# Kernel optimization log

Hardware: AMD Instinct MI355X
Metric: run time of the kernel (lower is better)

The kernel has to match this reference:

```python
import jax, jax.numpy as jnp
import numpy as np

N_GRIDS = 16
N_FEATS = 2
GRID_SHAPE = (64, 64, 64)  # D, H, W
NODES = 64
N_OUT = 1
DATA_MIN = 0.0
DATA_MAX = 1.0
N_POINTS = 524288


def setup_inputs() -> dict:
    key = jax.random.key(0)
    ks = jax.random.split(key, 12)
    x = jax.random.uniform(ks[0], (N_POINTS, 3), jnp.float32, -1.0, 1.0)
    # matches randomize_grids(): scales ~ log(1 - U*0.05), rotations ~ identity quat + noise,
    # translations ~ U(-0.05, 0.05)
    scales = jnp.log(1.0 - jax.random.uniform(ks[1], (N_GRIDS, 3), jnp.float32) * 0.05)
    rotations = jnp.zeros((N_GRIDS, 4), jnp.float32).at[:, 3].set(1.0) \
        + jax.random.normal(ks[2], (N_GRIDS, 4), jnp.float32) * 0.05
    translations = jax.random.uniform(ks[3], (N_GRIDS, 3), jnp.float32) * 0.1 - 0.05
    # original uses U(-1e-4, 1e-4); use a larger scale for numerically meaningful outputs
    feature_grids = jax.random.uniform(ks[4], (N_GRIDS, N_FEATS) + GRID_SHAPE,
                                       jnp.float32, -0.1, 0.1)
    d_in = N_GRIDS * N_FEATS
    def xavier(k, fi, fo):
        std = np.sqrt(2.0 / (fi + fo)).astype(np.float32)
        return jax.random.normal(k, (fi, fo), jnp.float32) * std
    W0 = xavier(ks[5], d_in, NODES)
    b0 = jax.random.normal(ks[6], (NODES,), jnp.float32) * 0.001
    W1 = xavier(ks[7], NODES, NODES)
    b1 = jax.random.normal(ks[8], (NODES,), jnp.float32) * 0.001
    W2 = xavier(ks[9], NODES, N_OUT)
    b2 = jax.random.normal(ks[10], (N_OUT,), jnp.float32) * 0.001
    return {"x": x, "rotations": rotations, "scales": scales,
            "translations": translations, "feature_grids": feature_grids,
            "W0": W0, "b0": b0, "W1": W1, "b1": b1, "W2": W2, "b2": b2}


def quat_to_rot(q):
    # q: [G,4] in (x, y, z, w) order; normalized (rotation_activation)
    q = q / jnp.linalg.norm(q, axis=-1, keepdims=True)
    x, y, z, w = q[:, 0], q[:, 1], q[:, 2], q[:, 3]
    r0 = jnp.stack([1 - 2 * (y * y + z * z), 2 * (x * y - z * w), 2 * (x * z + y * w)], -1)
    r1 = jnp.stack([2 * (x * y + z * w), 1 - 2 * (x * x + z * z), 2 * (y * z - x * w)], -1)
    r2 = jnp.stack([2 * (x * z - y * w), 2 * (y * z + x * w), 1 - 2 * (x * x + y * y)], -1)
    return jnp.stack([r0, r1, r2], axis=-2)  # [G,3,3]


def transform_points(x, rotations, scales, translations):
    # S*R*T order: local = diag(exp(scales)) @ R @ x + t, per grid -> [G,N,3]
    R = quat_to_rot(rotations)
    s = jnp.exp(scales)
    M = s[:, :, None] * R  # [G,3,3]
    return jnp.einsum('gij,nj->gni', M, x) + translations[:, None, :]


def trilinear_sample(grid, pts):
    # grid: [C,D,H,W]; pts: [N,3] (x,y,z) in [-1,1]; grid_sample semantics:
    # mode='bilinear', align_corners=True, padding_mode='zeros'
    C, D, H, W = grid.shape
    fx = (pts[:, 0] + 1.0) * 0.5 * (W - 1)
    fy = (pts[:, 1] + 1.0) * 0.5 * (H - 1)
    fz = (pts[:, 2] + 1.0) * 0.5 * (D - 1)
    x0 = jnp.floor(fx); y0 = jnp.floor(fy); z0 = jnp.floor(fz)
    wx = fx - x0; wy = fy - y0; wz = fz - z0
    x0i = x0.astype(jnp.int32); y0i = y0.astype(jnp.int32); z0i = z0.astype(jnp.int32)

    def corner(dx, dy, dz):
        xi = x0i + dx; yi = y0i + dy; zi = z0i + dz
        valid = (xi >= 0) & (xi < W) & (yi >= 0) & (yi < H) & (zi >= 0) & (zi < D)
        v = grid[:, jnp.clip(zi, 0, D - 1), jnp.clip(yi, 0, H - 1), jnp.clip(xi, 0, W - 1)]
        w = ((wx if dx else 1 - wx) * (wy if dy else 1 - wy) * (wz if dz else 1 - wz))
        return v * jnp.where(valid, w, 0.0)[None, :]

    out = corner(0, 0, 0)
    for dz in (0, 1):
        for dy in (0, 1):
            for dx in (0, 1):
                if (dx, dy, dz) != (0, 0, 0):
                    out = out + corner(dx, dy, dz)
    return out  # [C,N]


def reference(x, rotations, scales, translations, feature_grids, W0, b0, W1, b1, W2, b2):
    pts = transform_points(x, rotations, scales, translations)      # [G,N,3]
    feats = jax.vmap(trilinear_sample)(feature_grids, pts)          # [G,C,N]
    feats = feats.transpose(2, 0, 1).reshape(x.shape[0], -1)        # [N, G*C]
    h = jax.nn.relu(feats @ W0 + b0)
    h = jax.nn.relu(h @ W1 + b1)
    y = h @ W2 + b2
    return y * (DATA_MAX - DATA_MIN) + DATA_MIN
```

## Files before the change

### kernel.cpp

```cpp
#include <hip/hip_runtime.h>
#include <cstddef>
#include <cstdint>

constexpr int NPTS   = 524288;
constexpr int NG     = 16;
constexpr int GR     = 64;
constexpr int GR3    = GR * GR * GR;
constexpr int NNODES = 64;
constexpr int NBINS  = 32768;

constexpr size_t GRIDS_BYTES = (size_t)NG * GR3 * 8;
constexpr size_t WS_SORT     = GRIDS_BYTES;
constexpr size_t SORT_BYTES  = (size_t)NPTS * 16;
constexpr size_t WS_KEYR     = WS_SORT + SORT_BYTES;
constexpr size_t KEYR_BYTES  = (size_t)NPTS * 4;
constexpr size_t WS_BINS     = WS_KEYR + KEYR_BYTES;
constexpr size_t BINS_BYTES  = (size_t)NBINS * 4;
constexpr size_t WS_MATS     = WS_BINS + BINS_BYTES;
constexpr size_t MATS_BYTES  = 1024;
constexpr size_t WS_WPACK    = WS_MATS + MATS_BYTES;
constexpr size_t WPACK_BYTES = (size_t)(256 + 512) * 16;
constexpr size_t WS_TOTAL    = WS_WPACK + WPACK_BYTES;

constexpr int PREP_REPACK = 4096;
constexpr int PREP_HIST   = 2048;

typedef _Float16 half8 __attribute__((ext_vector_type(8)));
typedef float    floatx4 __attribute__((ext_vector_type(4)));

__device__ __forceinline__ unsigned part1by2(unsigned x) {
    x &= 0x3ff;
    x = (x | (x << 16)) & 0x030000FF;
    x = (x | (x <<  8)) & 0x0300F00F;
    x = (x | (x <<  4)) & 0x030C30C3;
    x = (x | (x <<  2)) & 0x09249249;
    return x;
}

__device__ __forceinline__ unsigned cell_of(float px, float py, float pz) {
    int cx = (int)((px + 1.0f) * 16.0f); cx = min(max(cx, 0), 31);
    int cy = (int)((py + 1.0f) * 16.0f); cy = min(max(cy, 0), 31);
    int cz = (int)((pz + 1.0f) * 16.0f); cz = min(max(cz, 0), 31);
    return part1by2((unsigned)cx) | (part1by2((unsigned)cy) << 1) | (part1by2((unsigned)cz) << 2);
}

__device__ __forceinline__ unsigned f32_to_bf16_rne(float f) {
    unsigned u = __float_as_uint(f);
    return (u + 0x7fffu + ((u >> 16) & 1u)) >> 16;
}

__device__ __forceinline__ unsigned pack_h2(float a, float b) {
    unsigned short ua = __builtin_bit_cast(unsigned short, (_Float16)a);
    unsigned short ub = __builtin_bit_cast(unsigned short, (_Float16)b);
    return (unsigned)ua | ((unsigned)ub << 16);
}

__global__ __launch_bounds__(256) void prep_kernel(
    const float* __restrict__ grids, uint2* __restrict__ gout,
    const float* __restrict__ xs, unsigned* __restrict__ bins,
    unsigned* __restrict__ keyrank,
    const float* __restrict__ rot, const float* __restrict__ scl,
    const float* __restrict__ trn, float* __restrict__ mats,
    const float* __restrict__ W0, const float* __restrict__ W1,
    uint4* __restrict__ wpack)
{
    const int bid = blockIdx.x;
    const int tid = threadIdx.x;

    if (bid < PREP_REPACK) {
        const int base = (bid * 256 + tid) * 4;
        const int g    = base >> 18;
        const int node = base & (GR3 - 1);
        const int x    = node & 63;
        const float* p0 = grids + (size_t)g * 2 * GR3 + node;
        const float* p1 = p0 + GR3;
        const float4 c0 = *(const float4*)p0;
        const float4 c1 = *(const float4*)p1;
        float d0n, d1n;
        if (x == 60) { d0n = c0.w; d1n = c1.w; }
        else         { d0n = p0[4]; d1n = p1[4]; }
        const float e0[5] = {c0.x, c0.y, c0.z, c0.w, d0n};
        const float e1[5] = {c1.x, c1.y, c1.z, c1.w, d1n};
        unsigned pk[5];
        #pragma unroll
        for (int i = 0; i < 5; ++i)
            pk[i] = f32_to_bf16_rne(e0[i]) | (f32_to_bf16_rne(e1[i]) << 16);
        uint4* dst = (uint4*)(gout + (size_t)g * GR3 + node);
        dst[0] = make_uint4(pk[0], pk[1], pk[1], pk[2]);
        dst[1] = make_uint4(pk[2], pk[3], pk[3], pk[4]);
    } else if (bid < PREP_REPACK + PREP_HIST) {
        const int n = (bid - PREP_REPACK) * 256 + tid;
        const unsigned key = cell_of(xs[n*3+0], xs[n*3+1], xs[n*3+2]);
        const unsigned rank = atomicAdd(&bins[key], 1u);
        keyrank[n] = key | (rank << 15);
    } else if (bid == PREP_REPACK + PREP_HIST) {
        const int g = tid;
        if (g < NG) {
            float qx = rot[g*4+0], qy = rot[g*4+1], qz = rot[g*4+2], qw = rot[g*4+3];
            const float inv = 1.0f / sqrtf(qx*qx + qy*qy + qz*qz + qw*qw);
            qx *= inv; qy *= inv; qz *= inv; qw *= inv;
            const float sx = expf(scl[g*3+0]);
            const float sy = expf(scl[g*3+1]);
            const float sz = expf(scl[g*3+2]);
            float* m = mats + g * 12;
            m[0] = sx * (1.0f - 2.0f*(qy*qy + qz*qz));
            m[1] = sx * (2.0f*(qx*qy - qz*qw));
            m[2] = sx * (2.0f*(qx*qz + qy*qw));
            m[3] = sy * (2.0f*(qx*qy + qz*qw));
            m[4] = sy * (1.0f - 2.0f*(qx*qx + qz*qz));
            m[5] = sy * (2.0f*(qy*qz - qx*qw));
            m[6] = sz * (2.0f*(qx*qz - qy*qw));
            m[7] = sz * (2.0f*(qy*qz + qx*qw));
            m[8] = sz * (1.0f - 2.0f*(qx*qx + qy*qy));
            m[9]  = trn[g*3+0];
            m[10] = trn[g*3+1];
            m[11] = trn[g*3+2];
        }
    } else {
        const int t = tid >> 6;
        const int lane = tid & 63;
        const int q = lane >> 4, c = lane & 15;
        const int n = t * 16 + c;
        {
            unsigned u[4];
            #pragma unroll
            for (int jj = 0; jj < 4; ++jj) {
                const int k0 = q * 8 + 2 * jj;
                u[jj] = pack_h2(W0[k0 * NNODES + n], W0[(k0 + 1) * NNODES + n]);
            }
            wpack[t * 64 + lane] = make_uint4(u[0], u[1], u[2], u[3]);
        }
        #pragma unroll
        for (int ks = 0; ks < 2; ++ks) {
            unsigned u[4];
            #pragma unroll
            for (int jj = 0; jj < 4; ++jj) {
                const int k0 = ks * 32 + q * 8 + 2 * jj;
                u[jj] = pack_h2(W1[k0 * NNODES + n], W1[(k0 + 1) * NNODES + n]);
            }
            wpack[256 + (ks * 4 + t) * 64 + lane] = make_uint4(u[0], u[1], u[2], u[3]);
        }
    }
}

__global__ __launch_bounds__(1024) void scan_kernel(unsigned* __restrict__ bins) {
    __shared__ unsigned s[1024];
    const int t = threadIdx.x;
    unsigned loc[32];
    unsigned sum = 0;
    #pragma unroll
    for (int i = 0; i < 32; ++i) { loc[i] = bins[t * 32 + i]; sum += loc[i]; }
    s[t] = sum;
    __syncthreads();
    for (int off = 1; off < 1024; off <<= 1) {
        unsigned v = (t >= off) ? s[t - off] : 0u;
        __syncthreads();
        s[t] += v;
        __syncthreads();
    }
    unsigned run = s[t] - sum;
    #pragma unroll
    for (int i = 0; i < 32; ++i) { bins[t * 32 + i] = run; run += loc[i]; }
}

__global__ __launch_bounds__(256) void scatter_kernel(const float* __restrict__ xs,
                                                      const unsigned* __restrict__ bins,
                                                      const unsigned* __restrict__ keyrank,
                                                      float4* __restrict__ sorted) {
    const int n = blockIdx.x * 256 + threadIdx.x;
    if (n >= NPTS) return;
    const unsigned kr = keyrank[n];
    const unsigned key = kr & 0x7fffu;
    const unsigned rank = kr >> 15;
    const unsigned pos = bins[key] + rank;
    sorted[pos] = make_float4(xs[n*3+0], xs[n*3+1], xs[n*3+2], __int_as_float(n));
}

struct Geom {
    int i00, i01, i10, i11;
    float ax0, ax1, ay0, ay1, az0, az1;
    unsigned selhi, sello;
};

__device__ __forceinline__ Geom make_geom(const float* __restrict__ m,
                                          float px, float py, float pz, int g) {
    Geom G;
    const float tx = fmaf(m[0], px, fmaf(m[1], py, fmaf(m[2], pz, m[9])));
    const float ty = fmaf(m[3], px, fmaf(m[4], py, fmaf(m[5], pz, m[10])));
    const float tz = fmaf(m[6], px, fmaf(m[7], py, fmaf(m[8], pz, m[11])));
    const float fx = (tx + 1.0f) * 31.5f;
    const float fy = (ty + 1.0f) * 31.5f;
    const float fz = (tz + 1.0f) * 31.5f;
    const float x0f = floorf(fx), y0f = floorf(fy), z0f = floorf(fz);
    const float wx = fx - x0f, wy = fy - y0f, wz = fz - z0f;
    const int x0 = (int)x0f, y0 = (int)y0f, z0 = (int)z0f;
    G.ax0 = ((unsigned)x0       < 64u) ? (1.0f - wx) : 0.0f;
    G.ax1 = ((unsigned)(x0 + 1) < 64u) ? wx          : 0.0f;
    G.ay0 = ((unsigned)y0       < 64u) ? (1.0f - wy) : 0.0f;
    G.ay1 = ((unsigned)(y0 + 1) < 64u) ? wy          : 0.0f;
    G.az0 = ((unsigned)z0       < 64u) ? (1.0f - wz) : 0.0f;
    G.az1 = ((unsigned)(z0 + 1) < 64u) ? wz          : 0.0f;
    G.selhi = (x0 >= 63) ? 1u : 0u;
    G.sello = (x0 <= -1) ? 1u : 0u;
    const int xb  = min(max(x0, 0), 62);
    const int yc0 = min(max(y0, 0), 63),     yc1 = min(max(y0 + 1, 0), 63);
    const int zc0 = min(max(z0, 0), 63),     zc1 = min(max(z0 + 1, 0), 63);
    const int b = (g << 18) + xb;
    G.i00 = b + (zc0 << 12) + (yc0 << 6);
    G.i01 = b + (zc0 << 12) + (yc1 << 6);
    G.i10 = b + (zc1 << 12) + (yc0 << 6);
    G.i11 = b + (zc1 << 12) + (yc1 << 6);
    return G;
}

__device__ __forceinline__ void acc_pair(float& f0, float& f1, const Geom& G,
                                         uint2 q, float wyz) {
    const unsigned v0 = G.selhi ? q.y : q.x;
    const unsigned v1 = G.sello ? q.x : q.y;
    float s0 = G.ax0 * __uint_as_float(v0 << 16);
    s0 = fmaf(G.ax1, __uint_as_float(v1 << 16), s0);
    f0 = fmaf(wyz, s0, f0);
    float s1 = G.ax0 * __uint_as_float(v0 & 0xffff0000u);
    s1 = fmaf(G.ax1, __uint_as_float(v1 & 0xffff0000u), s1);
    f1 = fmaf(wyz, s1, f1);
}

constexpr int ARENA_H = 64 * 66;
constexpr int FSTRIDE = 40;

__global__ __launch_bounds__(256, 4) void amgsrn_main(
    const float4* __restrict__ sorted,
    const uint2*  __restrict__ gridsP,
    const float*  __restrict__ mats,
    const uint4*  __restrict__ wpack,
    const float*  __restrict__ b0,
    const float*  __restrict__ b1,
    const float*  __restrict__ W2,
    const float*  __restrict__ b2,
    float* __restrict__ out)
{
    __shared__ unsigned short sh[4 * ARENA_H];
    __shared__ float yS[256];

    const int tid  = threadIdx.x;
    const int lane = tid & 63;
    const int wv   = tid >> 6;
    const int c    = lane & 15;
    const int q    = lane >> 4;
    unsigned short* wa = sh + wv * ARENA_H;

    const int n = blockIdx.x * 256 + tid;
    const float4 p = sorted[n];
    const float px = p.x, py = p.y, pz = p.z;
    const int orig = __float_as_int(p.w);

    unsigned pk[NG];
    Geom G = make_geom(mats, px, py, pz, 0);
    uint2 q00 = gridsP[G.i00], q01 = gridsP[G.i01];
    uint2 q10 = gridsP[G.i10], q11 = gridsP[G.i11];
    #pragma unroll
    for (int g = 0; g < NG; ++g) {
        Geom Gn;
        uint2 n00, n01, n10, n11;
        if (g + 1 < NG) {
            Gn = make_geom(mats + (g + 1) * 12, px, py, pz, g + 1);
            n00 = gridsP[Gn.i00]; n01 = gridsP[Gn.i01];
            n10 = gridsP[Gn.i10]; n11 = gridsP[Gn.i11];
        }
        float f0 = 0.0f, f1 = 0.0f;
        acc_pair(f0, f1, G, q00, G.az0 * G.ay0);
        acc_pair(f0, f1, G, q01, G.az0 * G.ay1);
        acc_pair(f0, f1, G, q10, G.az1 * G.ay0);
        acc_pair(f0, f1, G, q11, G.az1 * G.ay1);
        pk[g] = pack_h2(f0, f1);
        if (g + 1 < NG) {
            G = Gn;
            q00 = n00; q01 = n01; q10 = n10; q11 = n11;
        }
    }

    {
        uint4* dst = (uint4*)(wa + lane * FSTRIDE);
        dst[0] = make_uint4(pk[0],  pk[1],  pk[2],  pk[3]);
        dst[1] = make_uint4(pk[4],  pk[5],  pk[6],  pk[7]);
        dst[2] = make_uint4(pk[8],  pk[9],  pk[10], pk[11]);
        dst[3] = make_uint4(pk[12], pk[13], pk[14], pk[15]);
    }
    __syncthreads();

    half8 a0[4];
    #pragma unroll
    for (int m = 0; m < 4; ++m)
        a0[m] = *(const half8*)(wa + (m * 16 + c) * FSTRIDE + q * 8);

    half8 b0f[4], b1f[2][4];
    #pragma unroll
    for (int t = 0; t < 4; ++t)
        b0f[t] = __builtin_bit_cast(half8, wpack[t * 64 + lane]);
    #pragma unroll
    for (int ks = 0; ks < 2; ++ks)
        #pragma unroll
        for (int t = 0; t < 4; ++t)
            b1f[ks][t] = __builtin_bit_cast(half8, wpack[256 + (ks * 4 + t) * 64 + lane]);
    float b0v[4], b1v[4], w2v[4];
    #pragma unroll
    for (int t = 0; t < 4; ++t) {
        b0v[t] = b0[t * 16 + c];
        b1v[t] = b1[t * 16 + c];
        w2v[t] = W2[t * 16 + c];
    }
    const float b2s = b2[0];

    __syncthreads();

    #pragma unroll
    for (int t = 0; t < 4; ++t) {
        #pragma unroll
        for (int m = 0; m < 4; ++m) {
            floatx4 acc = {b0v[t], b0v[t], b0v[t], b0v[t]};
            acc = __builtin_amdgcn_mfma_f32_16x16x32_f16(a0[m], b0f[t], acc, 0, 0, 0);
            const int node = t * 16 + c;
            const int pt   = m * 16 + q * 4;
            unsigned* w32 = (unsigned*)(wa + node * 66 + pt);
            w32[0] = pack_h2(fmaxf(acc[0], 0.0f), fmaxf(acc[1], 0.0f));
            w32[1] = pack_h2(fmaxf(acc[2], 0.0f), fmaxf(acc[3], 0.0f));
        }
    }
    __syncthreads();

    half8 a1[4][2];
    #pragma unroll
    for (int m = 0; m < 4; ++m) {
        #pragma unroll
        for (int ks = 0; ks < 2; ++ks) {
            unsigned u[4];
            #pragma unroll
            for (int jj = 0; jj < 4; ++jj) {
                const int k0 = ks * 32 + q * 8 + 2 * jj;
                const unsigned lo = wa[k0 * 66 + m * 16 + c];
                const unsigned hi = wa[(k0 + 1) * 66 + m * 16 + c];
                u[jj] = lo | (hi << 16);
            }
            a1[m][ks] = __builtin_bit_cast(half8, make_uint4(u[0], u[1], u[2], u[3]));
        }
    }

    float p4[4][4];
    #pragma unroll
    for (int m = 0; m < 4; ++m)
        #pragma unroll
        for (int r = 0; r < 4; ++r) p4[m][r] = 0.0f;

    #pragma unroll
    for (int t = 0; t < 4; ++t) {
        #pragma unroll
        for (int m = 0; m < 4; ++m) {
            floatx4 acc = {b1v[t], b1v[t], b1v[t], b1v[t]};
            acc = __builtin_amdgcn_mfma_f32_16x16x32_f16(a1[m][0], b1f[0][t], acc, 0, 0, 0);
            acc = __builtin_amdgcn_mfma_f32_16x16x32_f16(a1[m][1], b1f[1][t], acc, 0, 0, 0);
            #pragma unroll
            for (int r = 0; r < 4; ++r)
                p4[m][r] = fmaf(fmaxf(acc[r], 0.0f), w2v[t], p4[m][r]);
        }
    }

    #pragma unroll
    for (int m = 0; m < 4; ++m)
        #pragma unroll
        for (int r = 0; r < 4; ++r) {
            float v = p4[m][r];
            v += __shfl_xor(v, 1, 64);
            v += __shfl_xor(v, 2, 64);
            v += __shfl_xor(v, 4, 64);
            v += __shfl_xor(v, 8, 64);
            p4[m][r] = v + b2s;
        }

    if (c == 0) {
        #pragma unroll
        for (int m = 0; m < 4; ++m)
            #pragma unroll
            for (int r = 0; r < 4; ++r)
                yS[wv * 64 + m * 16 + q * 4 + r] = p4[m][r];
    }
    __syncthreads();
    out[orig] = yS[tid];
}

__global__ __launch_bounds__(256, 3) void amgsrn_fused_fallback(
    const float* __restrict__ xs,
    const float* __restrict__ rot,
    const float* __restrict__ scl,
    const float* __restrict__ trn,
    const float* __restrict__ grids,
    const float* __restrict__ W0,
    const float* __restrict__ b0,
    const float* __restrict__ W1,
    const float* __restrict__ b1,
    const float* __restrict__ W2,
    const float* __restrict__ b2,
    float* __restrict__ out)
{
    __shared__ float sM[NG][12];
    const int tid = threadIdx.x;
    if (tid < NG) {
        const int g = tid;
        float qx = rot[g*4+0], qy = rot[g*4+1], qz = rot[g*4+2], qw = rot[g*4+3];
        const float inv = 1.0f / sqrtf(qx*qx + qy*qy + qz*qz + qw*qw);
        qx *= inv; qy *= inv; qz *= inv; qw *= inv;
        const float sx = expf(scl[g*3+0]);
        const float sy = expf(scl[g*3+1]);
        const float sz = expf(scl[g*3+2]);
        sM[g][0] = sx * (1.0f - 2.0f*(qy*qy + qz*qz));
        sM[g][1] = sx * (2.0f*(qx*qy - qz*qw));
        sM[g][2] = sx * (2.0f*(qx*qz + qy*qw));
        sM[g][3] = sy * (2.0f*(qx*qy + qz*qw));
        sM[g][4] = sy * (1.0f - 2.0f*(qx*qx + qz*qz));
        sM[g][5] = sy * (2.0f*(qy*qz - qx*qw));
        sM[g][6] = sz * (2.0f*(qx*qz - qy*qw));
        sM[g][7] = sz * (2.0f*(qy*qz + qx*qw));
        sM[g][8] = sz * (1.0f - 2.0f*(qx*qx + qy*qy));
        sM[g][9]  = trn[g*3+0];
        sM[g][10] = trn[g*3+1];
        sM[g][11] = trn[g*3+2];
    }
    __syncthreads();

    const int n = blockIdx.x * blockDim.x + tid;
    if (n >= NPTS) return;
    const float px = xs[n*3+0];
    const float py = xs[n*3+1];
    const float pz = xs[n*3+2];

    float h0[NNODES];
    #pragma unroll
    for (int j = 0; j < NNODES; ++j) h0[j] = b0[j];

    #pragma unroll
    for (int g = 0; g < NG; ++g) {
        const float* m = sM[g];
        const float tx = m[0]*px + m[1]*py + m[2]*pz + m[9];
        const float ty = m[3]*px + m[4]*py + m[5]*pz + m[10];
        const float tz = m[6]*px + m[7]*py + m[8]*pz + m[11];
        const float fx = (tx + 1.0f) * 31.5f;
        const float fy = (ty + 1.0f) * 31.5f;
        const float fz = (tz + 1.0f) * 31.5f;
        const float x0f = floorf(fx), y0f = floorf(fy), z0f = floorf(fz);
        const float wx = fx - x0f, wy = fy - y0f, wz = fz - z0f;
        const int x0 = (int)x0f, y0 = (int)y0f, z0 = (int)z0f;
        const float* gb = grids + (size_t)g * (size_t)(2 * GR3);
        float f0 = 0.0f, f1 = 0.0f;
        #pragma unroll
        for (int dz = 0; dz < 2; ++dz) {
            #pragma unroll
            for (int dy = 0; dy < 2; ++dy) {
                #pragma unroll
                for (int dx = 0; dx < 2; ++dx) {
                    const int xi = x0 + dx, yi = y0 + dy, zi = z0 + dz;
                    const bool valid = ((unsigned)xi < (unsigned)GR) &
                                       ((unsigned)yi < (unsigned)GR) &
                                       ((unsigned)zi < (unsigned)GR);
                    const int xc = min(max(xi, 0), GR-1);
                    const int yc = min(max(yi, 0), GR-1);
                    const int zc = min(max(zi, 0), GR-1);
                    float w = (dx ? wx : 1.0f - wx) *
                              (dy ? wy : 1.0f - wy) *
                              (dz ? wz : 1.0f - wz);
                    w = valid ? w : 0.0f;
                    const int idx = (zc * GR + yc) * GR + xc;
                    f0 = fmaf(w, gb[idx], f0);
                    f1 = fmaf(w, gb[idx + GR3], f1);
                }
            }
        }
        const float* w0a = W0 + (2*g    ) * NNODES;
        const float* w0b = W0 + (2*g + 1) * NNODES;
        #pragma unroll
        for (int j = 0; j < NNODES; ++j)
            h0[j] = fmaf(f1, w0b[j], fmaf(f0, w0a[j], h0[j]));
    }
    #pragma unroll
    for (int j = 0; j < NNODES; ++j) h0[j] = fmaxf(h0[j], 0.0f);

    float y = b2[0];
    #pragma unroll
    for (int half = 0; half < 2; ++half) {
        float h1[32];
        #pragma unroll
        for (int j = 0; j < 32; ++j) h1[j] = b1[half * 32 + j];
        #pragma unroll
        for (int k = 0; k < NNODES; ++k) {
            const float a = h0[k];
            const float* w = W1 + k * NNODES + half * 32;
            #pragma unroll
            for (int j = 0; j < 32; ++j) h1[j] = fmaf(a, w[j], h1[j]);
        }
        #pragma unroll
        for (int j = 0; j < 32; ++j) y = fmaf(fmaxf(h1[j], 0.0f), W2[half * 32 + j], y);
    }

    out[n] = y;
}

extern "C" void kernel_launch(void* const* d_in, const int* in_sizes, int n_in,
                              void* d_out, int out_size, void* d_ws, size_t ws_size,
                              hipStream_t stream) {
    const float* xs  = (const float*)d_in[0];
    const float* rot = (const float*)d_in[1];
    const float* scl = (const float*)d_in[2];
    const float* trn = (const float*)d_in[3];
    const float* gr  = (const float*)d_in[4];
    const float* W0  = (const float*)d_in[5];
    const float* b0  = (const float*)d_in[6];
    const float* W1  = (const float*)d_in[7];
    const float* b1  = (const float*)d_in[8];
    const float* W2  = (const float*)d_in[9];
    const float* b2  = (const float*)d_in[10];
    float* out = (float*)d_out;

    if (ws_size < WS_TOTAL) {
        dim3 grid((NPTS + 255) / 256), block(256);
        hipLaunchKernelGGL(amgsrn_fused_fallback, grid, block, 0, stream,
                           xs, rot, scl, trn, gr, W0, b0, W1, b1, W2, b2, out);
        return;
    }

    char* ws = (char*)d_ws;
    uint2*    gridsP  = (uint2*)(ws);
    float4*   sorted  = (float4*)(ws + WS_SORT);
    unsigned* keyrank = (unsigned*)(ws + WS_KEYR);
    unsigned* bins    = (unsigned*)(ws + WS_BINS);
    float*    mats    = (float*)(ws + WS_MATS);
    uint4*    wpack   = (uint4*)(ws + WS_WPACK);

    hipMemsetAsync(bins, 0, BINS_BYTES, stream);
    hipLaunchKernelGGL(prep_kernel, dim3(PREP_REPACK + PREP_HIST + 2), dim3(256), 0, stream,
                       gr, gridsP, xs, bins, keyrank,
                       rot, scl, trn, mats, W0, W1, wpack);
    hipLaunchKernelGGL(scan_kernel, dim3(1), dim3(1024), 0, stream, bins);
    hipLaunchKernelGGL(scatter_kernel, dim3(NPTS / 256), dim3(256), 0, stream,
                       xs, bins, keyrank, sorted);
    hipLaunchKernelGGL(amgsrn_main, dim3(NPTS / 256), dim3(256), 0, stream,
                       sorted, gridsP, mats, wpack, b0, b1, W2, b2, out);
}
```

Measured before the change: 196.8 us.

## Parallelize bin scan, deepen grid-gather prefetch, transpose hidden-layer LDS layout

The single-block 1024-thread scan over the 32768 bins is split into a 128-block local scan, a tiny scan of the block partials, and a scatter that adds the partial offset. The main kernel's grid-corner gathers are now prefetched two grids ahead instead of one, so more global loads are in flight per thread. The layer-0 activations are stored point-major with a stride of 72, which lets layer-1 A fragments be read as single 16-byte vector loads instead of being assembled from scalar halves. The costs are one extra kernel launch, more live registers from the deeper prefetch (a risk to occupancy under launch bounds of 256,4), and scattered 16-bit LDS stores on the write side.

```diff
diff --git a/kernel.cpp b/kernel.cpp
--- a/kernel.cpp
+++ b/kernel.cpp
@@ -20,7 +20,9 @@
 constexpr size_t MATS_BYTES  = 1024;
 constexpr size_t WS_WPACK    = WS_MATS + MATS_BYTES;
 constexpr size_t WPACK_BYTES = (size_t)(256 + 512) * 16;
-constexpr size_t WS_TOTAL    = WS_WPACK + WPACK_BYTES;
+constexpr size_t WS_PART     = WS_WPACK + WPACK_BYTES;
+constexpr size_t PART_BYTES  = 128 * 4;
+constexpr size_t WS_TOTAL    = WS_PART + PART_BYTES;
 
 constexpr int PREP_REPACK = 4096;
 constexpr int PREP_HIST   = 2048;
@@ -53,6 +55,10 @@
     unsigned short ua = __builtin_bit_cast(unsigned short, (_Float16)a);
     unsigned short ub = __builtin_bit_cast(unsigned short, (_Float16)b);
     return (unsigned)ua | ((unsigned)ub << 16);
+}
+
+__device__ __forceinline__ unsigned short f32_to_h16(float a) {
+    return __builtin_bit_cast(unsigned short, (_Float16)a);
 }
 
 __global__ __launch_bounds__(256) void prep_kernel(
@@ -143,28 +149,42 @@
     }
 }
 
-__global__ __launch_bounds__(1024) void scan_kernel(unsigned* __restrict__ bins) {
-    __shared__ unsigned s[1024];
+__global__ __launch_bounds__(256) void scanA_kernel(unsigned* __restrict__ bins,
+                                                    unsigned* __restrict__ part) {
+    __shared__ unsigned s[256];
     const int t = threadIdx.x;
-    unsigned loc[32];
-    unsigned sum = 0;
-    #pragma unroll
-    for (int i = 0; i < 32; ++i) { loc[i] = bins[t * 32 + i]; sum += loc[i]; }
-    s[t] = sum;
-    __syncthreads();
-    for (int off = 1; off < 1024; off <<= 1) {
-        unsigned v = (t >= off) ? s[t - off] : 0u;
+    const int base = blockIdx.x * 256;
+    const unsigned v = bins[base + t];
+    s[t] = v;
+    __syncthreads();
+    for (int off = 1; off < 256; off <<= 1) {
+        unsigned u = (t >= off) ? s[t - off] : 0u;
         __syncthreads();
-        s[t] += v;
+        s[t] += u;
         __syncthreads();
     }
-    unsigned run = s[t] - sum;
-    #pragma unroll
-    for (int i = 0; i < 32; ++i) { bins[t * 32 + i] = run; run += loc[i]; }
+    bins[base + t] = s[t] - v;
+    if (t == 255) part[blockIdx.x] = s[255];
+}
+
+__global__ __launch_bounds__(128) void scanB_kernel(unsigned* __restrict__ part) {
+    __shared__ unsigned s[128];
+    const int t = threadIdx.x;
+    const unsigned v = part[t];
+    s[t] = v;
+    __syncthreads();
+    for (int off = 1; off < 128; off <<= 1) {
+        unsigned u = (t >= off) ? s[t - off] : 0u;
+        __syncthreads();
+        s[t] += u;
+        __syncthreads();
+    }
+    part[t] = s[t] - v;
 }
 
 __global__ __launch_bounds__(256) void scatter_kernel(const float* __restrict__ xs,
                                                       const unsigned* __restrict__ bins,
+                                                      const unsigned* __restrict__ part,
                                                       const unsigned* __restrict__ keyrank,
                                                       float4* __restrict__ sorted) {
     const int n = blockIdx.x * 256 + threadIdx.x;
@@ -172,7 +192,7 @@
     const unsigned kr = keyrank[n];
     const unsigned key = kr & 0x7fffu;
     const unsigned rank = kr >> 15;
-    const unsigned pos = bins[key] + rank;
+    const unsigned pos = part[key >> 8] + bins[key] + rank;
     sorted[pos] = make_float4(xs[n*3+0], xs[n*3+1], xs[n*3+2], __int_as_float(n));
 }
 
@@ -225,7 +245,8 @@
     f1 = fmaf(wyz, s1, f1);
 }
 
-constexpr int ARENA_H = 64 * 66;
+constexpr int HSTR    = 72;
+constexpr int ARENA_H = 64 * HSTR;
 constexpr int FSTRIDE = 40;
 
 __global__ __launch_bounds__(256, 4) void amgsrn_main(
@@ -255,27 +276,30 @@
     const int orig = __float_as_int(p.w);
 
     unsigned pk[NG];
-    Geom G = make_geom(mats, px, py, pz, 0);
-    uint2 q00 = gridsP[G.i00], q01 = gridsP[G.i01];
-    uint2 q10 = gridsP[G.i10], q11 = gridsP[G.i11];
+    Geom Ga = make_geom(mats, px, py, pz, 0);
+    uint2 a00 = gridsP[Ga.i00], a01 = gridsP[Ga.i01];
+    uint2 a10 = gridsP[Ga.i10], a11 = gridsP[Ga.i11];
+    Geom Gb = make_geom(mats + 12, px, py, pz, 1);
+    uint2 b00 = gridsP[Gb.i00], b01 = gridsP[Gb.i01];
+    uint2 b10 = gridsP[Gb.i10], b11 = gridsP[Gb.i11];
     #pragma unroll
     for (int g = 0; g < NG; ++g) {
         Geom Gn;
         uint2 n00, n01, n10, n11;
-        if (g + 1 < NG) {
-            Gn = make_geom(mats + (g + 1) * 12, px, py, pz, g + 1);
+        if (g + 2 < NG) {
+            Gn = make_geom(mats + (g + 2) * 12, px, py, pz, g + 2);
             n00 = gridsP[Gn.i00]; n01 = gridsP[Gn.i01];
             n10 = gridsP[Gn.i10]; n11 = gridsP[Gn.i11];
         }
         float f0 = 0.0f, f1 = 0.0f;
-        acc_pair(f0, f1, G, q00, G.az0 * G.ay0);
-        acc_pair(f0, f1, G, q01, G.az0 * G.ay1);
-        acc_pair(f0, f1, G, q10, G.az1 * G.ay0);
-        acc_pair(f0, f1, G, q11, G.az1 * G.ay1);
+        acc_pair(f0, f1, Ga, a00, Ga.az0 * Ga.ay0);
+        acc_pair(f0, f1, Ga, a01, Ga.az0 * Ga.ay1);
+        acc_pair(f0, f1, Ga, a10, Ga.az1 * Ga.ay0);
+        acc_pair(f0, f1, Ga, a11, Ga.az1 * Ga.ay1);
         pk[g] = pack_h2(f0, f1);
-        if (g + 1 < NG) {
-            G = Gn;
-            q00 = n00; q01 = n01; q10 = n10; q11 = n11;
+        Ga = Gb; a00 = b00; a01 = b01; a10 = b10; a11 = b11;
+        if (g + 2 < NG) {
+            Gb = Gn; b00 = n00; b01 = n01; b10 = n10; b11 = n11;
         }
     }
 
@@ -320,30 +344,20 @@
             floatx4 acc = {b0v[t], b0v[t], b0v[t], b0v[t]};
             acc = __builtin_amdgcn_mfma_f32_16x16x32_f16(a0[m], b0f[t], acc, 0, 0, 0);
             const int node = t * 16 + c;
-            const int pt   = m * 16 + q * 4;
-            unsigned* w32 = (unsigned*)(wa + node * 66 + pt);
-            w32[0] = pack_h2(fmaxf(acc[0], 0.0f), fmaxf(acc[1], 0.0f));
-            w32[1] = pack_h2(fmaxf(acc[2], 0.0f), fmaxf(acc[3], 0.0f));
+            const int ptb  = m * 16 + q * 4;
+            #pragma unroll
+            for (int r = 0; r < 4; ++r)
+                wa[(ptb + r) * HSTR + node] = f32_to_h16(fmaxf(acc[r], 0.0f));
         }
     }
     __syncthreads();
 
     half8 a1[4][2];
     #pragma unroll
-    for (int m = 0; m < 4; ++m) {
-        #pragma unroll
-        for (int ks = 0; ks < 2; ++ks) {
-            unsigned u[4];
-            #pragma unroll
-            for (int jj = 0; jj < 4; ++jj) {
-                const int k0 = ks * 32 + q * 8 + 2 * jj;
-                const unsigned lo = wa[k0 * 66 + m * 16 + c];
-                const unsigned hi = wa[(k0 + 1) * 66 + m * 16 + c];
-                u[jj] = lo | (hi << 16);
-            }
-            a1[m][ks] = __builtin_bit_cast(half8, make_uint4(u[0], u[1], u[2], u[3]));
-        }
-    }
+    for (int m = 0; m < 4; ++m)
+        #pragma unroll
+        for (int ks = 0; ks < 2; ++ks)
+            a1[m][ks] = *(const half8*)(wa + (m * 16 + c) * HSTR + ks * 32 + q * 8);
 
     float p4[4][4];
     #pragma unroll
@@ -532,14 +546,16 @@
     unsigned* bins    = (unsigned*)(ws + WS_BINS);
     float*    mats    = (float*)(ws + WS_MATS);
     uint4*    wpack   = (uint4*)(ws + WS_WPACK);
+    unsigned* part    = (unsigned*)(ws + WS_PART);
 
     hipMemsetAsync(bins, 0, BINS_BYTES, stream);
     hipLaunchKernelGGL(prep_kernel, dim3(PREP_REPACK + PREP_HIST + 2), dim3(256), 0, stream,
                        gr, gridsP, xs, bins, keyrank,
                        rot, scl, trn, mats, W0, W1, wpack);
-    hipLaunchKernelGGL(scan_kernel, dim3(1), dim3(1024), 0, stream, bins);
+    hipLaunchKernelGGL(scanA_kernel, dim3(NBINS / 256), dim3(256), 0, stream, bins, part);
+    hipLaunchKernelGGL(scanB_kernel, dim3(1), dim3(128), 0, stream, part);
     hipLaunchKernelGGL(scatter_kernel, dim3(NPTS / 256), dim3(256), 0, stream,
-                       xs, bins, keyrank, sorted);
+                       xs, bins, part, keyrank, sorted);
     hipLaunchKernelGGL(amgsrn_main, dim3(NPTS / 256), dim3(256), 0, stream,
                        sorted, gridsP, mats, wpack, b0, b1, W2, b2, out);
 }
```

After: 189.2 us. -3.9%, faster.
